# Optimization experiments

Hardware: AMD Instinct MI355X
Metric: run time of the kernel (lower is better)

## Reference

```python
import jax, jax.numpy as jnp
import numpy as np

FEAT_STRIDE = 16
PRE_NMS = 6000
POST_NMS = 300
NMS_THRESH = 0.7


def _whctrs(a):
    w = a[2] - a[0] + 1.0
    h = a[3] - a[1] + 1.0
    return w, h, a[0] + 0.5 * (w - 1), a[1] + 0.5 * (h - 1)

def _mkanchors(ws, hs, xc, yc):
    return np.stack([xc - 0.5 * (ws - 1), yc - 0.5 * (hs - 1),
                     xc + 0.5 * (ws - 1), yc + 0.5 * (hs - 1)], axis=1)

def _ratio_enum(anchor, ratios):
    w, h, xc, yc = _whctrs(anchor)
    size = w * h
    ws = np.round(np.sqrt(size / ratios))
    hs = np.round(ws * ratios)
    return _mkanchors(ws, hs, xc, yc)

def _scale_enum(anchor, scales):
    w, h, xc, yc = _whctrs(anchor)
    return _mkanchors(w * scales, h * scales, xc, yc)

def generate_anchors(base_size=16, ratios=np.array([0.5, 1.0, 2.0]), scales=np.array([8, 16, 32])):
    base = np.array([1, 1, base_size, base_size], dtype=np.float64) - 1
    ra = _ratio_enum(base, np.asarray(ratios, np.float64))
    return np.vstack([_scale_enum(ra[i], np.asarray(scales, np.float64)) for i in range(ra.shape[0])])


def setup_inputs() -> dict:
    key = jax.random.key(0)
    k1, k2 = jax.random.split(key)
    B, A, H, W = 8, 9, 64, 64
    scores = jax.random.normal(k1, (B, 2 * A, H, W), jnp.float32)
    bbox_deltas = jax.random.normal(k2, (B, 4 * A, H, W), jnp.float32)
    anchors = jnp.asarray(generate_anchors(16), jnp.float32)  # [9, 4]
    return {"scores": scores, "bbox_deltas": bbox_deltas, "anchors": anchors,
            "image_width": 1024, "image_height": 1024}


def _nms_keep(iou, thresh):
    # greedy NMS on score-sorted boxes given a full IoU matrix
    n = iou.shape[0]
    idx = jnp.arange(n)
    def body(i, keep):
        sup = keep[i] & (iou[i] > thresh) & (idx > i)
        return keep & ~sup
    return jax.lax.fori_loop(0, n, body, jnp.ones((n,), bool))


def _nms_one(boxes):  # boxes [PRE_NMS, 4], sorted by score desc
    b = jax.lax.stop_gradient(boxes)
    area = (b[:, 2] - b[:, 0] + 1.0) * (b[:, 3] - b[:, 1] + 1.0)
    iw = jnp.clip(jnp.minimum(b[:, None, 2], b[None, :, 2]) -
                  jnp.maximum(b[:, None, 0], b[None, :, 0]) + 1.0, 0.0)
    ih = jnp.clip(jnp.minimum(b[:, None, 3], b[None, :, 3]) -
                  jnp.maximum(b[:, None, 1], b[None, :, 1]) + 1.0, 0.0)
    inter = iw * ih
    iou = inter / (area[:, None] + area[None, :] - inter)
    keep = _nms_keep(iou, NMS_THRESH)
    # compact kept boxes to the front, pad with zeros (fixed shape)
    rank = jnp.cumsum(keep) - 1
    dest = jnp.where(keep, rank, PRE_NMS)  # suppressed -> dump row
    out = jnp.zeros((PRE_NMS + 1, 4), boxes.dtype).at[dest].set(boxes)
    return out[:POST_NMS]


def _forward(scores, bbox_deltas, anchors, image_width, image_height):
    B = scores.shape[0]
    A = anchors.shape[0]
    H, W = scores.shape[2], scores.shape[3]
    fg = scores[:, A:, :, :]                                   # [B, A, H, W]
    # shifted anchor grid
    mx, my = jnp.meshgrid(jnp.arange(W) * FEAT_STRIDE, jnp.arange(H) * FEAT_STRIDE)
    shifts = jnp.stack([mx.ravel(), my.ravel(), mx.ravel(), my.ravel()], 1).astype(scores.dtype)
    all_anchors = (shifts[:, None, :] + anchors[None, :, :]).reshape(-1, 4)  # [K*A, 4]
    deltas = bbox_deltas.transpose(0, 2, 3, 1).reshape(B, -1, 4)             # [B, K*A, 4]
    sc = fg.transpose(0, 2, 3, 1).reshape(B, -1)                             # [B, K*A]
    # bbox_transform_inv
    aw = all_anchors[:, 2] - all_anchors[:, 0] + 1.0
    ah = all_anchors[:, 3] - all_anchors[:, 1] + 1.0
    acx = all_anchors[:, 0] + 0.5 * aw
    acy = all_anchors[:, 1] + 0.5 * ah
    pcx = deltas[..., 0] * aw + acx
    pcy = deltas[..., 1] * ah + acy
    pw = jnp.exp(deltas[..., 2]) * aw
    ph = jnp.exp(deltas[..., 3]) * ah
    # clip to image
    x1 = jnp.clip(pcx - 0.5 * pw, 0.0, image_width - 1)
    y1 = jnp.clip(pcy - 0.5 * ph, 0.0, image_height - 1)
    x2 = jnp.clip(pcx + 0.5 * pw, 0.0, image_width - 1)
    y2 = jnp.clip(pcy + 0.5 * ph, 0.0, image_height - 1)
    proposals = jnp.stack([x1, y1, x2, y2], -1)                 # [B, K*A, 4]
    # per-image pre-NMS top-k by score
    _, order = jax.lax.top_k(sc, PRE_NMS)
    boxes = jnp.take_along_axis(proposals, order[..., None], axis=1)  # [B, PRE, 4]
    props = jax.lax.map(_nms_one, boxes)                        # [B, POST, 4]
    bidx = jnp.broadcast_to(jnp.arange(B, dtype=props.dtype)[:, None, None], (B, POST_NMS, 1))
    return jnp.concatenate([bidx, props], axis=-1)              # [B, POST, 5]


def reference(scores, bbox_deltas, anchors, image_width, image_height):
    return _forward(scores, bbox_deltas, anchors, image_width, image_height)
```

## Files before the change

### kernel.cpp

```cpp
#include <hip/hip_runtime.h>
#include <math.h>

#pragma clang fp contract(off)

#define BB 8
#define AA 9
#define NPIX 4096
#define NN (NPIX*AA)
#define PRE 6000
#define POST 300
#define SELCAP 7000
#define HWORDS 16384
#define TMAX 10111

#define RA 0x3F000000u
#define RB 0x41000000u
__device__ __forceinline__ unsigned key_bin(unsigned k) {
    unsigned bin;
    if (k < RA)      bin = k >> 17;
    else if (k < RB) bin = 8064u + ((k - RA) >> 14);
    else             bin = 10112u + ((k - RB) >> 17);
    return (bin > 32767u) ? 32767u : bin;
}

#define SMEM_BYTES 65536

__device__ __forceinline__ unsigned score_key(float s) {
    unsigned fb = __float_as_uint(s);
    unsigned u = (fb & 0x80000000u) ? ~fb : (fb | 0x80000000u);
    return ~u;
}

__device__ __forceinline__ unsigned phalf(unsigned v, unsigned bin) {
    return (v >> ((bin & 1) << 4)) & 0xFFFFu;
}

__device__ __forceinline__ bool iou_gt(float ax1, float ay1, float ax2, float ay2, float aa,
                                       float bx1_, float by1_, float bx2_, float by2_, float ab) {
    float xx1 = fmaxf(ax1, bx1_);
    float yy1 = fmaxf(ay1, by1_);
    float xx2 = fminf(ax2, bx2_);
    float yy2 = fminf(ay2, by2_);
    float iw = fmaxf(xx2 - xx1 + 1.0f, 0.0f);
    float ih = fmaxf(yy2 - yy1 + 1.0f, 0.0f);
    float inter = iw * ih;
    float uni = (aa + ab) - inter;
    return (double)inter >= 0x1.666667p-1 * (double)uni;
}

__device__ __forceinline__ void decode_box(int g, const unsigned short* sorted16,
                                           const float* anch, const float* deltas_b,
                                           float fw, float fh, float4* bx, float* ar) {
    unsigned idx = sorted16[(g < PRE) ? g : (PRE - 1)];
    int a = (int)(idx % AA);
    int pix = (int)(idx / AA);
    int wq = pix & 63, hq = pix >> 6;
    float sx = (float)(wq * 16), sy = (float)(hq * 16);
    float ax1 = anch[a * 4 + 0] + sx, ay1 = anch[a * 4 + 1] + sy;
    float ax2 = anch[a * 4 + 2] + sx, ay2 = anch[a * 4 + 3] + sy;
    float aw = ax2 - ax1 + 1.0f, ah = ay2 - ay1 + 1.0f;
    float acx = ax1 + 0.5f * aw, acy = ay1 + 0.5f * ah;
    const float* dp = deltas_b + (size_t)(a * 4) * NPIX + pix;
    float d0 = dp[0], d1 = dp[NPIX], d2 = dp[2 * NPIX], d3 = dp[3 * NPIX];
    float pcx = d0 * aw + acx, pcy = d1 * ah + acy;
    float pw = expf(d2) * aw, ph = expf(d3) * ah;
    float x1 = fminf(fmaxf(pcx - 0.5f * pw, 0.0f), fw);
    float y1 = fminf(fmaxf(pcy - 0.5f * ph, 0.0f), fh);
    float x2 = fminf(fmaxf(pcx + 0.5f * pw, 0.0f), fw);
    float y2 = fminf(fmaxf(pcy + 0.5f * ph, 0.0f), fh);
    *bx = make_float4(x1, y1, x2, y2);
    *ar = (x2 - x1 + 1.0f) * (y2 - y1 + 1.0f);
}

__global__ __launch_bounds__(1024) void proposal_kernel(const float* __restrict__ scores,
                                                        const float* __restrict__ deltas,
                                                        const float* __restrict__ anchors,
                                                        const int* __restrict__ imw,
                                                        const int* __restrict__ imh,
                                                        float* __restrict__ out) {
    __shared__ __align__(16) unsigned char smem[SMEM_BYTES];
    unsigned*       hist32 = (unsigned*)smem;
    unsigned*       keyh   = (unsigned*)(smem + 20480);
    unsigned short* idxl   = (unsigned short*)(smem + 48512);
    unsigned*       scal   = (unsigned*)(smem + 65344);
    unsigned short* sorted16 = (unsigned short*)(smem + 20480);
    float4*         kb4  = (float4*)smem;
    float*          kba  = (float*)(smem + 4800);
    float4*         cnd4 = (float4*)(smem + 6016);
    float*          cnda = (float*)(smem + 8064);
    unsigned long long* srow  = (unsigned long long*)(smem + 8576);
    unsigned long long* deadw = (unsigned long long*)(smem + 9088);
    float*          anch = (float*)(smem + 9216);

    int b = blockIdx.x;
    int tid = threadIdx.x;
    int wave = tid >> 6, lane = tid & 63;
    const float* sc = scores + (size_t)(b * (2 * AA) + AA) * NPIX;
    const float* deltas_b = deltas + (size_t)b * (4 * AA) * NPIX;
    float fw = (float)(imw[0] - 1);
    float fh = (float)(imh[0] - 1);

    for (int j = tid; j < HWORDS; j += 1024) hist32[j] = 0;
    __syncthreads();
    #pragma unroll
    for (int q = 0; q < 36; ++q) {
        unsigned bin = key_bin(score_key(sc[tid + (q << 10)]));
        atomicAdd(&hist32[bin >> 1], 1u << ((bin & 1) << 4));
    }
    __syncthreads();

    const unsigned* hw = hist32 + tid * 16;
    unsigned ssum = 0;
    #pragma unroll
    for (int j = 0; j < 16; ++j) { unsigned w = hw[j]; ssum += (w & 0xFFFFu) + (w >> 16); }
    __syncthreads();
    unsigned x = ssum;
    #pragma unroll
    for (int d = 1; d < 64; d <<= 1) {
        unsigned y = __shfl_up(x, (unsigned)d, 64);
        if (lane >= d) x += y;
    }
    if (lane == 63) scal[wave] = x;
    __syncthreads();
    unsigned wexcl = 0;
    #pragma unroll
    for (int w = 0; w < 16; ++w) if (w < wave) wexcl += scal[w];
    unsigned gexcl = wexcl + (x - ssum);
    unsigned gincl = gexcl + ssum;
    if (gexcl <= (PRE - 1) && (PRE - 1) < gincl) {
        unsigned c = gexcl, T = tid * 32, tot = gincl;
        bool f = false;
        for (int j = 0; j < 32 && !f; ++j) {
            unsigned d = phalf(hw[j >> 1], (unsigned)j);
            if ((PRE - 1) < c + d) { T = tid * 32 + j; tot = c + d; f = true; }
            c += d;
        }
        scal[16] = T;
        scal[17] = tot;
    }
    __syncthreads();
    unsigned T = scal[16];
    if (T > TMAX) T = TMAX;
    unsigned cnt = scal[17];
    if (cnt > SELCAP) cnt = SELCAP;

    if ((unsigned)(tid * 32) <= T) {
        unsigned run = gexcl;
        unsigned* wv = hist32 + tid * 16;
        #pragma unroll
        for (int j = 0; j < 16; ++j) {
            unsigned v = wv[j];
            unsigned c0 = v & 0xFFFFu, c1 = v >> 16;
            wv[j] = run | ((run + c0) << 16);
            run += c0 + c1;
        }
    }
    __syncthreads();

    #pragma unroll
    for (int q = 0; q < 36; ++q) {
        int r = (q << 10) + tid;
        unsigned k = score_key(sc[r]);
        unsigned bin = key_bin(k);
        if (bin <= T) {
            unsigned old = atomicAdd(&hist32[bin >> 1], 1u << ((bin & 1) << 4));
            unsigned pos = phalf(old, bin);
            if (pos < SELCAP) {
                keyh[pos] = k;
                int a = r >> 12, pix = r & 4095;
                idxl[pos] = (unsigned short)(pix * AA + a);
            }
        }
    }
    __syncthreads();

    unsigned rnk8[8], id8[8];
    #pragma unroll
    for (int m = 0; m < 8; ++m) {
        int s = (m << 10) + tid;
        rnk8[m] = 0xFFFFFFFFu;
        if (s < (int)cnt) {
            unsigned k = keyh[s];
            unsigned id = idxl[s];
            unsigned bin = key_bin(k);
            unsigned start = bin ? phalf(hist32[(bin - 1) >> 1], bin - 1) : 0u;
            unsigned end = phalf(hist32[bin >> 1], bin);
            if (end > cnt) end = cnt;
            if (start > end) start = end;
            unsigned rank = start;
            for (unsigned j = start; j < end; ++j) {
                unsigned kj = keyh[j];
                if (kj < k) ++rank;
                else if (kj == k) rank += ((unsigned)idxl[j] < id) ? 1u : 0u;
            }
            rnk8[m] = rank;
            id8[m] = id;
        }
    }
    __syncthreads();
    #pragma unroll
    for (int m = 0; m < 8; ++m)
        if (rnk8[m] < PRE) sorted16[rnk8[m]] = (unsigned short)id8[m];
    if (tid < 36) anch[tid] = anchors[tid];
    __syncthreads();

    if (tid < 64) {
        float4 bx; float ar;
        decode_box(tid, sorted16, anch, deltas_b, fw, fh, &bx, &ar);
        cnd4[tid] = bx; cnda[tid] = ar;
    }
    __syncthreads();

    int cur = 0, K = 0, p = 0;
    for (;;) {
        float4 mc = cnd4[p * 64 + lane];
        float ma = cnda[p * 64 + lane];

        float4 nb; float na;
        if (wave == 8)
            decode_box(cur + 64 + lane, sorted16, anch, deltas_b, fw, fh, &nb, &na);

        bool dead = (cur + lane >= PRE);
        for (int k = wave; k < K; k += 16) {
            float4 kv = kb4[k];
            float ka = kba[k];
            dead = dead || iou_gt(kv.x, kv.y, kv.z, kv.w, ka, mc.x, mc.y, mc.z, mc.w, ma);
        }
        unsigned long long db = __ballot(dead);
        if (lane == 0) deadw[wave] = db;

        #pragma unroll
        for (int q2 = 0; q2 < 4; ++q2) {
            int j = (q2 << 4) + wave;
            float4 cj = cnd4[p * 64 + j];
            float aj = cnda[p * 64 + j];
            bool g = (lane < j) && iou_gt(mc.x, mc.y, mc.z, mc.w, ma,
                                          cj.x, cj.y, cj.z, cj.w, aj);
            unsigned long long bl = __ballot(g);
            if (lane == 0) srow[j] = bl;
        }
        if (wave == 8) {
            cnd4[(p ^ 1) * 64 + lane] = nb;
            cnda[(p ^ 1) * 64 + lane] = na;
        }
        __syncthreads();

        unsigned long long dk = deadw[0];
        #pragma unroll
        for (int w = 1; w < 16; ++w) dk |= deadw[w];
        unsigned long long row = srow[lane];
        unsigned long long live = ~dk;
        unsigned long long keptb = 0ULL;
        int allowed = POST - K;
        while (live) {
            int f = __ffsll((long long)live) - 1;
            keptb |= (1ULL << f);
            if (__popcll(keptb) >= allowed) break;
            bool die = (row >> f) & 1ULL;
            unsigned long long dbl = __ballot(die);
            live &= ~(dbl | (1ULL << f));
        }
        int nkeep = __popcll(keptb);
        int take = (nkeep < allowed) ? nkeep : allowed;

        if (wave == 0 && ((keptb >> lane) & 1ULL)) {
            int rnk = __popcll(keptb & ((1ULL << lane) - 1ULL));
            if (rnk < take) { kb4[K + rnk] = mc; kba[K + rnk] = ma; }
        }
        K += take;
        cur += 64;
        if (K >= POST || cur >= PRE) break;
        p ^= 1;
        __syncthreads();
    }

    __syncthreads();
    for (int idx = tid; idx < POST * 5; idx += 1024) {
        int row_ = idx / 5;
        int col = idx - row_ * 5;
        float val = 0.0f;
        if (row_ < K) {
            float4 v = kb4[row_];
            val = (col == 0) ? (float)b : (col == 1) ? v.x : (col == 2) ? v.y
                : (col == 3) ? v.z : v.w;
        }
        out[(size_t)b * POST * 5 + idx] = val;
    }
}

extern "C" void kernel_launch(void* const* d_in, const int* in_sizes, int n_in,
                              void* d_out, int out_size, void* d_ws, size_t ws_size,
                              hipStream_t stream) {
    const float* scores  = (const float*)d_in[0];
    const float* deltas  = (const float*)d_in[1];
    const float* anchors = (const float*)d_in[2];
    const int*   imw     = (const int*)d_in[3];
    const int*   imh     = (const int*)d_in[4];
    float* out = (float*)d_out;

    proposal_kernel<<<BB, 1024, 0, stream>>>(scores, deltas, anchors, imw, imh, out);
}
```

Before: 161.1 us.

## Split top-k selection across 256 cooperative blocks with grid syncs

Replaces the one-block-per-image kernel with a cooperative launch of 256 blocks, 32 per image. Histogramming, bin scatter, rank computation and box decoding now run across all blocks using global-memory histograms and workspace arrays, separated by grid-wide syncs. Eight blocks then run the NMS loop from pre-decoded boxes, and intra-chunk IoU work is skipped when every candidate in a chunk is already dead. This brings more CUs to the selection phase but adds a memset, four grid barriers and global atomics and traffic in place of LDS.

```diff
diff --git a/kernel.cpp b/kernel.cpp
--- a/kernel.cpp
+++ b/kernel.cpp
@@ -1,7 +1,10 @@
 #include <hip/hip_runtime.h>
+#include <hip/hip_cooperative_groups.h>
 #include <math.h>
 
 #pragma clang fp contract(off)
+
+namespace cg = cooperative_groups;
 
 #define BB 8
 #define AA 9
@@ -9,9 +12,15 @@
 #define NN (NPIX*AA)
 #define PRE 6000
 #define POST 300
-#define SELCAP 7000
-#define HWORDS 16384
-#define TMAX 10111
+#define SELCAP 8192
+#define NBINS 32768
+
+#define GH_OFF    0ULL
+#define BINFO_OFF 1048576ULL
+#define SELK_OFF  1048640ULL
+#define BARR_OFF  1572928ULL
+#define AARR_OFF  2340928ULL
+#define ZERO_BYTES (1048576ULL + 64ULL)
 
 #define RA 0x3F000000u
 #define RB 0x41000000u
@@ -23,16 +32,10 @@
     return (bin > 32767u) ? 32767u : bin;
 }
 
-#define SMEM_BYTES 65536
-
 __device__ __forceinline__ unsigned score_key(float s) {
     unsigned fb = __float_as_uint(s);
     unsigned u = (fb & 0x80000000u) ? ~fb : (fb | 0x80000000u);
     return ~u;
-}
-
-__device__ __forceinline__ unsigned phalf(unsigned v, unsigned bin) {
-    return (v >> ((bin & 1) << 4)) & 0xFFFFu;
 }
 
 __device__ __forceinline__ bool iou_gt(float ax1, float ay1, float ax2, float ay2, float aa,
@@ -48,167 +51,157 @@
     return (double)inter >= 0x1.666667p-1 * (double)uni;
 }
 
-__device__ __forceinline__ void decode_box(int g, const unsigned short* sorted16,
-                                           const float* anch, const float* deltas_b,
-                                           float fw, float fh, float4* bx, float* ar) {
-    unsigned idx = sorted16[(g < PRE) ? g : (PRE - 1)];
-    int a = (int)(idx % AA);
-    int pix = (int)(idx / AA);
-    int wq = pix & 63, hq = pix >> 6;
-    float sx = (float)(wq * 16), sy = (float)(hq * 16);
-    float ax1 = anch[a * 4 + 0] + sx, ay1 = anch[a * 4 + 1] + sy;
-    float ax2 = anch[a * 4 + 2] + sx, ay2 = anch[a * 4 + 3] + sy;
-    float aw = ax2 - ax1 + 1.0f, ah = ay2 - ay1 + 1.0f;
-    float acx = ax1 + 0.5f * aw, acy = ay1 + 0.5f * ah;
-    const float* dp = deltas_b + (size_t)(a * 4) * NPIX + pix;
-    float d0 = dp[0], d1 = dp[NPIX], d2 = dp[2 * NPIX], d3 = dp[3 * NPIX];
-    float pcx = d0 * aw + acx, pcy = d1 * ah + acy;
-    float pw = expf(d2) * aw, ph = expf(d3) * ah;
-    float x1 = fminf(fmaxf(pcx - 0.5f * pw, 0.0f), fw);
-    float y1 = fminf(fmaxf(pcy - 0.5f * ph, 0.0f), fh);
-    float x2 = fminf(fmaxf(pcx + 0.5f * pw, 0.0f), fw);
-    float y2 = fminf(fmaxf(pcy + 0.5f * ph, 0.0f), fh);
-    *bx = make_float4(x1, y1, x2, y2);
-    *ar = (x2 - x1 + 1.0f) * (y2 - y1 + 1.0f);
-}
-
 __global__ __launch_bounds__(1024) void proposal_kernel(const float* __restrict__ scores,
                                                         const float* __restrict__ deltas,
                                                         const float* __restrict__ anchors,
                                                         const int* __restrict__ imw,
                                                         const int* __restrict__ imh,
-                                                        float* __restrict__ out) {
-    __shared__ __align__(16) unsigned char smem[SMEM_BYTES];
-    unsigned*       hist32 = (unsigned*)smem;
-    unsigned*       keyh   = (unsigned*)(smem + 20480);
-    unsigned short* idxl   = (unsigned short*)(smem + 48512);
-    unsigned*       scal   = (unsigned*)(smem + 65344);
-    unsigned short* sorted16 = (unsigned short*)(smem + 20480);
-    float4*         kb4  = (float4*)smem;
-    float*          kba  = (float*)(smem + 4800);
-    float4*         cnd4 = (float4*)(smem + 6016);
-    float*          cnda = (float*)(smem + 8064);
-    unsigned long long* srow  = (unsigned long long*)(smem + 8576);
-    unsigned long long* deadw = (unsigned long long*)(smem + 9088);
-    float*          anch = (float*)(smem + 9216);
-
-    int b = blockIdx.x;
+                                                        float* __restrict__ out,
+                                                        unsigned* __restrict__ ghist,
+                                                        unsigned* __restrict__ binfo,
+                                                        unsigned long long* __restrict__ selk,
+                                                        float4* __restrict__ barr,
+                                                        float* __restrict__ aarr) {
+    cg::grid_group grid = cg::this_grid();
+    __shared__ unsigned wtot[16];
+    __shared__ unsigned tb[2];
+    __shared__ float4 kb4[POST];
+    __shared__ float  kba[POST];
+    __shared__ float4 cnd4[128];
+    __shared__ float  cnda[128];
+    __shared__ unsigned long long srow[64];
+    __shared__ unsigned long long deadw[16];
+
+    int bid = blockIdx.x;
     int tid = threadIdx.x;
     int wave = tid >> 6, lane = tid & 63;
+    int b = bid >> 5, sub = bid & 31;
     const float* sc = scores + (size_t)(b * (2 * AA) + AA) * NPIX;
-    const float* deltas_b = deltas + (size_t)b * (4 * AA) * NPIX;
-    float fw = (float)(imw[0] - 1);
-    float fh = (float)(imh[0] - 1);
-
-    for (int j = tid; j < HWORDS; j += 1024) hist32[j] = 0;
-    __syncthreads();
+    unsigned* gh = ghist + ((size_t)b << 15);
+
     #pragma unroll
-    for (int q = 0; q < 36; ++q) {
-        unsigned bin = key_bin(score_key(sc[tid + (q << 10)]));
-        atomicAdd(&hist32[bin >> 1], 1u << ((bin & 1) << 4));
-    }
-    __syncthreads();
-
-    const unsigned* hw = hist32 + tid * 16;
-    unsigned ssum = 0;
+    for (int i = 0; i < 2; ++i) {
+        int e = i * 1024 + tid;
+        if (e < 1152) {
+            int r = sub * 1152 + e;
+            unsigned bin = key_bin(score_key(sc[r]));
+            atomicAdd(&gh[bin], 1u);
+        }
+    }
+    grid.sync();
+
+    if (bid < BB) {
+        unsigned* g2 = ghist + ((size_t)bid << 15);
+        int base = tid * 32;
+        unsigned ssum = 0;
+        for (int j = 0; j < 32; ++j) ssum += g2[base + j];
+        unsigned x = ssum;
+        #pragma unroll
+        for (int d = 1; d < 64; d <<= 1) {
+            unsigned y = __shfl_up(x, (unsigned)d, 64);
+            if (lane >= d) x += y;
+        }
+        if (lane == 63) wtot[wave] = x;
+        __syncthreads();
+        unsigned wexcl = 0;
+        #pragma unroll
+        for (int w = 0; w < 16; ++w) if (w < wave) wexcl += wtot[w];
+        unsigned gexcl = wexcl + (x - ssum);
+        unsigned gincl = gexcl + ssum;
+        unsigned run = gexcl;
+        for (int j = 0; j < 32; ++j) {
+            unsigned c = g2[base + j];
+            g2[base + j] = run;
+            run += c;
+        }
+        if (gexcl <= (PRE - 1) && (PRE - 1) < gincl) {
+            unsigned c = gexcl, T = base, tot = gincl;
+            run = gexcl;
+            bool f = false;
+            for (int j = 0; j < 32 && !f; ++j) {
+                unsigned d = g2[base + j + 1 > base + 31 ? base + j : base + j];
+                (void)d;
+                unsigned lo = g2[base + j];
+                unsigned hi = (j < 31) ? g2[base + j + 1] : gincl;
+                unsigned cj = hi - lo;
+                if ((PRE - 1) < c + cj) { T = base + j; tot = c + cj; f = true; }
+                c += cj;
+            }
+            binfo[bid * 2 + 0] = T;
+            binfo[bid * 2 + 1] = tot;
+        }
+    }
+    grid.sync();
+
+    unsigned T = binfo[b * 2 + 0];
+    unsigned cnt = binfo[b * 2 + 1];
+    if (cnt > SELCAP) cnt = SELCAP;
+
     #pragma unroll
-    for (int j = 0; j < 16; ++j) { unsigned w = hw[j]; ssum += (w & 0xFFFFu) + (w >> 16); }
-    __syncthreads();
-    unsigned x = ssum;
-    #pragma unroll
-    for (int d = 1; d < 64; d <<= 1) {
-        unsigned y = __shfl_up(x, (unsigned)d, 64);
-        if (lane >= d) x += y;
-    }
-    if (lane == 63) scal[wave] = x;
-    __syncthreads();
-    unsigned wexcl = 0;
-    #pragma unroll
-    for (int w = 0; w < 16; ++w) if (w < wave) wexcl += scal[w];
-    unsigned gexcl = wexcl + (x - ssum);
-    unsigned gincl = gexcl + ssum;
-    if (gexcl <= (PRE - 1) && (PRE - 1) < gincl) {
-        unsigned c = gexcl, T = tid * 32, tot = gincl;
-        bool f = false;
-        for (int j = 0; j < 32 && !f; ++j) {
-            unsigned d = phalf(hw[j >> 1], (unsigned)j);
-            if ((PRE - 1) < c + d) { T = tid * 32 + j; tot = c + d; f = true; }
-            c += d;
-        }
-        scal[16] = T;
-        scal[17] = tot;
-    }
-    __syncthreads();
-    unsigned T = scal[16];
-    if (T > TMAX) T = TMAX;
-    unsigned cnt = scal[17];
-    if (cnt > SELCAP) cnt = SELCAP;
-
-    if ((unsigned)(tid * 32) <= T) {
-        unsigned run = gexcl;
-        unsigned* wv = hist32 + tid * 16;
-        #pragma unroll
-        for (int j = 0; j < 16; ++j) {
-            unsigned v = wv[j];
-            unsigned c0 = v & 0xFFFFu, c1 = v >> 16;
-            wv[j] = run | ((run + c0) << 16);
-            run += c0 + c1;
-        }
-    }
-    __syncthreads();
-
-    #pragma unroll
-    for (int q = 0; q < 36; ++q) {
-        int r = (q << 10) + tid;
-        unsigned k = score_key(sc[r]);
-        unsigned bin = key_bin(k);
-        if (bin <= T) {
-            unsigned old = atomicAdd(&hist32[bin >> 1], 1u << ((bin & 1) << 4));
-            unsigned pos = phalf(old, bin);
-            if (pos < SELCAP) {
-                keyh[pos] = k;
-                int a = r >> 12, pix = r & 4095;
-                idxl[pos] = (unsigned short)(pix * AA + a);
-            }
-        }
-    }
-    __syncthreads();
-
-    unsigned rnk8[8], id8[8];
-    #pragma unroll
-    for (int m = 0; m < 8; ++m) {
-        int s = (m << 10) + tid;
-        rnk8[m] = 0xFFFFFFFFu;
+    for (int i = 0; i < 2; ++i) {
+        int e = i * 1024 + tid;
+        if (e < 1152) {
+            int r = sub * 1152 + e;
+            unsigned k = score_key(sc[r]);
+            unsigned bin = key_bin(k);
+            if (bin <= T) {
+                unsigned pos = atomicAdd(&gh[bin], 1u);
+                if (pos < SELCAP) {
+                    int a = r >> 12, pix = r & 4095;
+                    selk[((size_t)b << 13) + pos] =
+                        ((unsigned long long)k << 32) | (unsigned)(pix * AA + a);
+                }
+            }
+        }
+    }
+    grid.sync();
+
+    {
+        int s = sub * 1024 + tid;
         if (s < (int)cnt) {
-            unsigned k = keyh[s];
-            unsigned id = idxl[s];
+            unsigned long long kv = selk[((size_t)b << 13) + s];
+            unsigned k = (unsigned)(kv >> 32);
             unsigned bin = key_bin(k);
-            unsigned start = bin ? phalf(hist32[(bin - 1) >> 1], bin - 1) : 0u;
-            unsigned end = phalf(hist32[bin >> 1], bin);
+            unsigned start = bin ? gh[bin - 1] : 0u;
+            unsigned end = gh[bin];
             if (end > cnt) end = cnt;
             if (start > end) start = end;
             unsigned rank = start;
-            for (unsigned j = start; j < end; ++j) {
-                unsigned kj = keyh[j];
-                if (kj < k) ++rank;
-                else if (kj == k) rank += ((unsigned)idxl[j] < id) ? 1u : 0u;
-            }
-            rnk8[m] = rank;
-            id8[m] = id;
-        }
-    }
-    __syncthreads();
-    #pragma unroll
-    for (int m = 0; m < 8; ++m)
-        if (rnk8[m] < PRE) sorted16[rnk8[m]] = (unsigned short)id8[m];
-    if (tid < 36) anch[tid] = anchors[tid];
-    __syncthreads();
-
-    if (tid < 64) {
-        float4 bx; float ar;
-        decode_box(tid, sorted16, anch, deltas_b, fw, fh, &bx, &ar);
-        cnd4[tid] = bx; cnda[tid] = ar;
-    }
+            for (unsigned j = start; j < end; ++j)
+                rank += (selk[((size_t)b << 13) + j] < kv) ? 1u : 0u;
+            if (rank < PRE) {
+                unsigned idx = (unsigned)(kv & 0xFFFFFFFFu);
+                int a = (int)(idx % AA);
+                int pix = (int)(idx / AA);
+                int wq = pix & 63, hq = pix >> 6;
+                float sx = (float)(wq * 16), sy = (float)(hq * 16);
+                float ax1 = anchors[a * 4 + 0] + sx, ay1 = anchors[a * 4 + 1] + sy;
+                float ax2 = anchors[a * 4 + 2] + sx, ay2 = anchors[a * 4 + 3] + sy;
+                float aw = ax2 - ax1 + 1.0f, ah = ay2 - ay1 + 1.0f;
+                float acx = ax1 + 0.5f * aw, acy = ay1 + 0.5f * ah;
+                const float* dp = deltas + ((size_t)b * (4 * AA) + (size_t)(a * 4)) * NPIX + pix;
+                float d0 = dp[0], d1 = dp[NPIX], d2 = dp[2 * NPIX], d3 = dp[3 * NPIX];
+                float pcx = d0 * aw + acx, pcy = d1 * ah + acy;
+                float pw = expf(d2) * aw, ph = expf(d3) * ah;
+                float fw = (float)(imw[0] - 1);
+                float fh = (float)(imh[0] - 1);
+                float x1 = fminf(fmaxf(pcx - 0.5f * pw, 0.0f), fw);
+                float y1 = fminf(fmaxf(pcy - 0.5f * ph, 0.0f), fh);
+                float x2 = fminf(fmaxf(pcx + 0.5f * pw, 0.0f), fw);
+                float y2 = fminf(fmaxf(pcy + 0.5f * ph, 0.0f), fh);
+                barr[(size_t)b * PRE + rank] = make_float4(x1, y1, x2, y2);
+                aarr[(size_t)b * PRE + rank] = (x2 - x1 + 1.0f) * (y2 - y1 + 1.0f);
+            }
+        }
+    }
+    grid.sync();
+
+    if (bid >= BB) return;
+    b = bid;
+    const float4* bxs = barr + (size_t)b * PRE;
+    const float* ars = aarr + (size_t)b * PRE;
+
+    if (tid < 64) { cnd4[tid] = bxs[tid]; cnda[tid] = ars[tid]; }
     __syncthreads();
 
     int cur = 0, K = 0, p = 0;
@@ -217,8 +210,10 @@
         float ma = cnda[p * 64 + lane];
 
         float4 nb; float na;
-        if (wave == 8)
-            decode_box(cur + 64 + lane, sorted16, anch, deltas_b, fw, fh, &nb, &na);
+        if (wave == 8) {
+            int g = cur + 64 + lane; if (g > PRE - 1) g = PRE - 1;
+            nb = bxs[g]; na = ars[g];
+        }
 
         bool dead = (cur + lane >= PRE);
         for (int k = wave; k < K; k += 16) {
@@ -228,17 +223,6 @@
         }
         unsigned long long db = __ballot(dead);
         if (lane == 0) deadw[wave] = db;
-
-        #pragma unroll
-        for (int q2 = 0; q2 < 4; ++q2) {
-            int j = (q2 << 4) + wave;
-            float4 cj = cnd4[p * 64 + j];
-            float aj = cnda[p * 64 + j];
-            bool g = (lane < j) && iou_gt(mc.x, mc.y, mc.z, mc.w, ma,
-                                          cj.x, cj.y, cj.z, cj.w, aj);
-            unsigned long long bl = __ballot(g);
-            if (lane == 0) srow[j] = bl;
-        }
         if (wave == 8) {
             cnd4[(p ^ 1) * 64 + lane] = nb;
             cnda[(p ^ 1) * 64 + lane] = na;
@@ -248,29 +232,47 @@
         unsigned long long dk = deadw[0];
         #pragma unroll
         for (int w = 1; w < 16; ++w) dk |= deadw[w];
-        unsigned long long row = srow[lane];
-        unsigned long long live = ~dk;
-        unsigned long long keptb = 0ULL;
-        int allowed = POST - K;
-        while (live) {
-            int f = __ffsll((long long)live) - 1;
-            keptb |= (1ULL << f);
-            if (__popcll(keptb) >= allowed) break;
-            bool die = (row >> f) & 1ULL;
-            unsigned long long dbl = __ballot(die);
-            live &= ~(dbl | (1ULL << f));
-        }
-        int nkeep = __popcll(keptb);
-        int take = (nkeep < allowed) ? nkeep : allowed;
-
-        if (wave == 0 && ((keptb >> lane) & 1ULL)) {
-            int rnk = __popcll(keptb & ((1ULL << lane) - 1ULL));
-            if (rnk < take) { kb4[K + rnk] = mc; kba[K + rnk] = ma; }
-        }
-        K += take;
+
+        if (dk != ~0ULL) {
+            #pragma unroll
+            for (int q2 = 0; q2 < 4; ++q2) {
+                int j = (q2 << 4) + wave;
+                if (!((dk >> j) & 1ULL)) {
+                    float4 cj = cnd4[p * 64 + j];
+                    float aj = cnda[p * 64 + j];
+                    bool g = (lane < j) && iou_gt(mc.x, mc.y, mc.z, mc.w, ma,
+                                                  cj.x, cj.y, cj.z, cj.w, aj);
+                    unsigned long long bl = __ballot(g);
+                    if (lane == 0) srow[j] = bl;
+                }
+            }
+            __syncthreads();
+
+            unsigned long long row = srow[lane];
+            unsigned long long live = ~dk;
+            unsigned long long keptb = 0ULL;
+            int allowed = POST - K;
+            while (live) {
+                int f = __ffsll((long long)live) - 1;
+                keptb |= (1ULL << f);
+                if (__popcll(keptb) >= allowed) break;
+                bool die = (row >> f) & 1ULL;
+                unsigned long long dbl = __ballot(die);
+                live &= ~(dbl | (1ULL << f));
+            }
+            int nkeep = __popcll(keptb);
+            int take = (nkeep < allowed) ? nkeep : allowed;
+
+            if (wave == 0 && ((keptb >> lane) & 1ULL)) {
+                int rnk = __popcll(keptb & ((1ULL << lane) - 1ULL));
+                if (rnk < take) { kb4[K + rnk] = mc; kba[K + rnk] = ma; }
+            }
+            K += take;
+        }
+
         cur += 64;
+        p ^= 1;
         if (K >= POST || cur >= PRE) break;
-        p ^= 1;
         __syncthreads();
     }
 
@@ -286,6 +288,7 @@
         }
         out[(size_t)b * POST * 5 + idx] = val;
     }
+    (void)tb; (void)wtot;
 }
 
 extern "C" void kernel_launch(void* const* d_in, const int* in_sizes, int n_in,
@@ -297,6 +300,20 @@
     const int*   imw     = (const int*)d_in[3];
     const int*   imh     = (const int*)d_in[4];
     float* out = (float*)d_out;
-
-    proposal_kernel<<<BB, 1024, 0, stream>>>(scores, deltas, anchors, imw, imh, out);
-}
+    char* ws = (char*)d_ws;
+
+    unsigned*           ghist = (unsigned*)(ws + GH_OFF);
+    unsigned*           binfo = (unsigned*)(ws + BINFO_OFF);
+    unsigned long long* selk  = (unsigned long long*)(ws + SELK_OFF);
+    float4*             barr  = (float4*)(ws + BARR_OFF);
+    float*              aarr  = (float*)(ws + AARR_OFF);
+
+    hipMemsetAsync(ws + GH_OFF, 0, ZERO_BYTES, stream);
+
+    void* args[] = { (void*)&scores, (void*)&deltas, (void*)&anchors,
+                     (void*)&imw, (void*)&imh, (void*)&out,
+                     (void*)&ghist, (void*)&binfo, (void*)&selk,
+                     (void*)&barr, (void*)&aarr };
+    hipLaunchCooperativeKernel((void*)proposal_kernel, dim3(256), dim3(1024),
+                               args, 0, stream);
+}
```

Result: slower. 299.6 us (+86.1%).
